# Performance work log

Measured on AMD Instinct MI355X. Metric: run time of the kernel, lower is better.

Reference implementation:

```python
import jax, jax.numpy as jnp
import numpy as np

HIDDEN = 2048
NUM_HEADS = 16
HEAD_DIM = 128
BLOCK_SIZE = 64
NUM_ACTIVE_BLOCKS = 4  # diagonal pattern -> bandwidth = 2 blocks each side
NEG_INF = -1e30  # stand-in for -inf that is safe under softmax in fp32


def _block_diagonal_additive_mask(seq_len: int) -> jnp.ndarray:
    """Token-level additive mask [S, S]; 0 where block |bi-bj|<=bandwidth, -inf else."""
    bandwidth = NUM_ACTIVE_BLOCKS // 2
    bid = jnp.arange(seq_len) // BLOCK_SIZE  # [S]
    active = jnp.abs(bid[:, None] - bid[None, :]) <= bandwidth  # [S, S] bool
    return jnp.where(active, 0.0, NEG_INF).astype(jnp.float32)


def setup_inputs() -> dict:
    key = jax.random.key(0)
    k0, k1, k2, k3, k4 = jax.random.split(key, 5)
    B, S = 2, 2048
    scale = 1.0 / np.sqrt(HIDDEN)
    return {
        "hidden_states": jax.random.normal(k0, (B, S, HIDDEN), dtype=jnp.float32),
        "Wq": jax.random.normal(k1, (HIDDEN, NUM_HEADS * HEAD_DIM), dtype=jnp.float32) * scale,
        "Wk": jax.random.normal(k2, (HIDDEN, NUM_HEADS * HEAD_DIM), dtype=jnp.float32) * scale,
        "Wv": jax.random.normal(k3, (HIDDEN, NUM_HEADS * HEAD_DIM), dtype=jnp.float32) * scale,
        "Wo": jax.random.normal(k4, (NUM_HEADS * HEAD_DIM, HIDDEN), dtype=jnp.float32) * scale,
    }


def reference(hidden_states, Wq, Wk, Wv, Wo):
    B, S, _ = hidden_states.shape
    scaling = HEAD_DIM ** -0.5

    # projections -> [B, H, S, D]
    def split_heads(x):
        return x.reshape(B, S, NUM_HEADS, HEAD_DIM).transpose(0, 2, 1, 3)

    q = split_heads(hidden_states @ Wq)
    k = split_heads(hidden_states @ Wk)
    v = split_heads(hidden_states @ Wv)

    mask = _block_diagonal_additive_mask(S)  # [S, S]

    # scores [B, H, S, S]
    scores = jnp.einsum("bhsd,bhtd->bhst", q, k) * scaling + mask[None, None]
    attn = jax.nn.softmax(scores.astype(jnp.float32), axis=-1).astype(q.dtype)

    out = jnp.einsum("bhst,bhtd->bhsd", attn, v)  # [B, H, S, D]
    out = out.transpose(0, 2, 1, 3).reshape(B, S, NUM_HEADS * HEAD_DIM)
    return out @ Wo
```

## Files before the change

kernel.cpp:

```cpp
#include <hip/hip_runtime.h>

typedef __attribute__((ext_vector_type(4))) float f32x4;
typedef __attribute__((ext_vector_type(16))) float f32x16;
typedef __attribute__((ext_vector_type(8))) _Float16 f16x8;
typedef __attribute__((ext_vector_type(4))) _Float16 f16x4;

__device__ __forceinline__ void gload_lds16(const void* g, void* l) {
  __builtin_amdgcn_global_load_lds((__attribute__((address_space(1))) void*)(g),
                                   (__attribute__((address_space(3))) void*)(l), 16, 0, 0);
}

#define BAR() asm volatile("s_barrier" ::: "memory")
#define WAITV8() asm volatile("s_waitcnt vmcnt(8)" ::: "memory")
#define WAITV6() asm volatile("s_waitcnt vmcnt(6)" ::: "memory")
#define WAITV4() asm volatile("s_waitcnt vmcnt(4)" ::: "memory")
#define WAITV0() asm volatile("s_waitcnt vmcnt(0)" ::: "memory")

__global__ __launch_bounds__(256) void prep(const float* __restrict__ Hs,
                                            const float* __restrict__ W0, const float* __restrict__ W1,
                                            const float* __restrict__ W2, const float* __restrict__ W3,
                                            _Float16* __restrict__ Hb, _Float16* __restrict__ Wt) {
  __shared__ _Float16 tile[64][65];
  const int bid = blockIdx.x, tid = threadIdx.x;
  if (bid < 8192) {
    int i = (bid * 256 + tid) * 4;
    float4 v = *(const float4*)(Hs + i);
    f16x4 o = { (_Float16)v.x, (_Float16)v.y, (_Float16)v.z, (_Float16)v.w };
    *(f16x4*)(Hb + i) = o;
    return;
  }
  const int t = bid - 8192;
  const int z = t >> 10, k0 = ((t >> 5) & 31) * 64, n0 = (t & 31) * 64;
  const float* W = z == 0 ? W0 : z == 1 ? W1 : z == 2 ? W2 : W3;
  _Float16* Wo_ = Wt + (size_t)z * (2048u * 2048u);
  #pragma unroll
  for (int p = 0; p < 4; ++p) {
    int o = p * 256 + tid, r = o >> 4, c = o & 15;
    float4 v = *(const float4*)(W + (size_t)(k0 + r) * 2048 + n0 + c * 4);
    tile[r][c * 4 + 0] = (_Float16)v.x;
    tile[r][c * 4 + 1] = (_Float16)v.y;
    tile[r][c * 4 + 2] = (_Float16)v.z;
    tile[r][c * 4 + 3] = (_Float16)v.w;
  }
  __syncthreads();
  #pragma unroll
  for (int p = 0; p < 2; ++p) {
    int o = p * 256 + tid, nl = o >> 3, c = o & 7;
    f16x8 u;
    #pragma unroll
    for (int i = 0; i < 8; ++i) u[i] = tile[c * 8 + i][nl];
    *(f16x8*)(Wo_ + (size_t)(n0 + nl) * 2048 + k0 + c * 8) = u;
  }
}

__device__ __forceinline__ void gemm256(const _Float16* __restrict__ A,
                                        const _Float16* __restrict__ Bt,
                                        _Float16* __restrict__ C, int ldc,
                                        int m0, int n0, _Float16* S) {
  _Float16* const As0 = S;
  _Float16* const As1 = S + 16384;
  _Float16* const Bs0 = S + 32768;
  _Float16* const Bs1 = S + 49152;
  const int tid = (int)threadIdx.x;
  const int lane = tid & 63, w = tid >> 6, l32 = lane & 31, half = lane >> 5;
  const int wm = (w & 1) * 128, wn = (w >> 1) * 64;

  f32x16 acc[4][2];
  #pragma unroll
  for (int s = 0; s < 4; ++s)
    #pragma unroll
    for (int t = 0; t < 2; ++t) acc[s][t] = 0;

  f16x8 af[2][4];
  f16x8 bf[2][4];

  auto stageA = [&](_Float16* dst, int ar, int kt) {
    const int r = tid >> 3, c = tid & 7;
    gload_lds16(A + (size_t)(m0 + ar + r) * 2048 + kt * 64 + ((c ^ (r & 7)) << 3),
                (char*)dst + ar * 128 + tid * 16);
  };
  auto stageB = [&](_Float16* dst, int br, int kt) {
    const int r = tid >> 3, c = tid & 7;
    gload_lds16(Bt + (size_t)(n0 + br + r) * 2048 + kt * 64 + ((c ^ (r & 7)) << 3),
                (char*)dst + br * 128 + tid * 16);
  };
  auto ldA = [&](const _Float16* as, int p) {
    #pragma unroll
    for (int s2 = 0; s2 < 2; ++s2)
      #pragma unroll
      for (int kk = 0; kk < 4; ++kk)
        af[s2][kk] = *(const f16x8*)(as + (wm + p * 64 + s2 * 32 + l32) * 64 +
                                     (((2 * kk + half) ^ (l32 & 7)) << 3));
  };
  auto ldB = [&](const _Float16* bs, int q) {
    #pragma unroll
    for (int kk = 0; kk < 4; ++kk)
      bf[q][kk] = *(const f16x8*)(bs + (wn + q * 32 + l32) * 64 +
                                  (((2 * kk + half) ^ (l32 & 7)) << 3));
  };
  auto mm8 = [&](int sp, int q) {
    __builtin_amdgcn_s_setprio(1);
    #pragma unroll
    for (int kk = 0; kk < 4; ++kk)
      #pragma unroll
      for (int s2 = 0; s2 < 2; ++s2)
        acc[sp * 2 + s2][q] = __builtin_amdgcn_mfma_f32_32x32x16_f16(
            bf[q][kk], af[s2][kk], acc[sp * 2 + s2][q], 0, 0, 0);
    __builtin_amdgcn_s_setprio(0);
  };

  stageA(As0, 0, 0); stageA(As0, 64, 0); stageA(As0, 128, 0); stageA(As0, 192, 0);
  stageB(Bs0, 0, 0); stageB(Bs0, 64, 0); stageB(Bs0, 128, 0); stageB(Bs0, 192, 0);
  stageA(As1, 0, 1); stageA(As1, 64, 1); stageA(As1, 128, 1); stageA(As1, 192, 1);
  stageB(Bs1, 0, 1); stageB(Bs1, 64, 1); stageB(Bs1, 128, 1); stageB(Bs1, 192, 1);
  WAITV8();
  BAR();

  auto tile = [&](int kt, _Float16* Ac, _Float16* Bc) {
    const bool g2 = (kt + 2) < 32;
    ldA(Ac, 0);
    ldB(Bc, 0); ldB(Bc, 1);
    mm8(0, 0);
    mm8(0, 1);
    ldA(Ac, 1);
    mm8(1, 1);
    mm8(1, 0);
    BAR();
    if (g2) {
      stageA(Ac, 0, kt + 2); stageA(Ac, 64, kt + 2);
      stageA(Ac, 128, kt + 2); stageA(Ac, 192, kt + 2);
      stageB(Bc, 0, kt + 2); stageB(Bc, 64, kt + 2);
      stageB(Bc, 128, kt + 2); stageB(Bc, 192, kt + 2);
      WAITV8();
    } else {
      WAITV0();
    }
    BAR();
  };

  #pragma unroll 1
  for (int kt = 0; kt < 32; kt += 2) {
    tile(kt, As0, Bs0);
    tile(kt + 1, As1, Bs1);
  }

  #pragma unroll
  for (int s = 0; s < 4; ++s) {
    const size_t row = (size_t)(wm + s * 32 + l32);
    #pragma unroll
    for (int t = 0; t < 2; ++t)
      #pragma unroll
      for (int g = 0; g < 4; ++g) {
        const int col = wn + t * 32 + g * 8 + 4 * half;
        f16x4 o = { (_Float16)acc[s][t][4 * g + 0], (_Float16)acc[s][t][4 * g + 1],
                    (_Float16)acc[s][t][4 * g + 2], (_Float16)acc[s][t][4 * g + 3] };
        *(f16x4*)(C + row * ldc + col) = o;
      }
  }
}

__device__ __forceinline__ void gemm128h(const _Float16* __restrict__ A,
                                         const _Float16* __restrict__ Bt,
                                         _Float16* __restrict__ C, int ldc,
                                         int m0, int n0, _Float16* S) {
  _Float16* const As0 = S;
  _Float16* const As1 = S + 8192;
  _Float16* const Bs0 = S + 16384;
  _Float16* const Bs1 = S + 32768;
  const int tid = (int)threadIdx.x;
  const int lane = tid & 63, w = tid >> 6, l32 = lane & 31, half = lane >> 5;
  const int wm = (w & 1) * 64, wn = (w >> 1) * 64;

  f32x16 acc[2][2];
  #pragma unroll
  for (int s = 0; s < 2; ++s)
    #pragma unroll
    for (int t = 0; t < 2; ++t) acc[s][t] = 0;

  f16x8 af[2][4], bf[2][4];

  auto stA = [&](_Float16* dst, int ar, int kt) {
    const int r = tid >> 3, c = tid & 7;
    gload_lds16(A + (size_t)(m0 + ar + r) * 2048 + kt * 64 + ((c ^ (r & 7)) << 3),
                (char*)dst + ar * 128 + tid * 16);
  };
  auto stB = [&](_Float16* dst, int br, int kt) {
    const int r = tid >> 3, c = tid & 7;
    gload_lds16(Bt + (size_t)(n0 + br + r) * 2048 + kt * 64 + ((c ^ (r & 7)) << 3),
                (char*)dst + br * 128 + tid * 16);
  };
  auto ldAq = [&](const _Float16* as) {
    #pragma unroll
    for (int s2 = 0; s2 < 2; ++s2)
      #pragma unroll
      for (int kk = 0; kk < 4; ++kk)
        af[s2][kk] = *(const f16x8*)(as + (wm + s2 * 32 + l32) * 64 +
                                     (((2 * kk + half) ^ (l32 & 7)) << 3));
  };
  auto ldBq = [&](const _Float16* bs, int q) {
    #pragma unroll
    for (int kk = 0; kk < 4; ++kk)
      bf[q][kk] = *(const f16x8*)(bs + (wn + q * 32 + l32) * 64 +
                                  (((2 * kk + half) ^ (l32 & 7)) << 3));
  };
  auto mmq = [&](int q) {
    __builtin_amdgcn_s_setprio(1);
    #pragma unroll
    for (int kk = 0; kk < 4; ++kk)
      #pragma unroll
      for (int s2 = 0; s2 < 2; ++s2)
        acc[s2][q] = __builtin_amdgcn_mfma_f32_32x32x16_f16(
            bf[q][kk], af[s2][kk], acc[s2][q], 0, 0, 0);
    __builtin_amdgcn_s_setprio(0);
  };

  stA(As0, 0, 0); stA(As0, 64, 0);
  stB(Bs0, 0, 0); stB(Bs0, 64, 0); stB(Bs0, 128, 0); stB(Bs0, 192, 0);
  stA(As1, 0, 1); stA(As1, 64, 1);
  stB(Bs1, 0, 1); stB(Bs1, 64, 1); stB(Bs1, 128, 1); stB(Bs1, 192, 1);
  WAITV6();
  BAR();

  auto tile = [&](int kt, _Float16* Ac, _Float16* Bc) {
    const bool g2 = (kt + 2) < 32;
    ldAq(Ac); ldBq(Bc, 0); ldBq(Bc, 1);
    mmq(0);
    mmq(1);
    BAR();
    if (g2) {
      stA(Ac, 0, kt + 2); stA(Ac, 64, kt + 2);
      stB(Bc, 0, kt + 2); stB(Bc, 64, kt + 2); stB(Bc, 128, kt + 2); stB(Bc, 192, kt + 2);
      WAITV6();
    } else {
      WAITV0();
    }
    BAR();
  };

  #pragma unroll 1
  for (int kt = 0; kt < 32; kt += 2) {
    tile(kt, As0, Bs0);
    tile(kt + 1, As1, Bs1);
  }

  #pragma unroll
  for (int s = 0; s < 2; ++s) {
    const size_t row = (size_t)(wm + s * 32 + l32);
    #pragma unroll
    for (int t = 0; t < 2; ++t)
      #pragma unroll
      for (int g = 0; g < 4; ++g) {
        const int col = wn + t * 32 + g * 8 + 4 * half;
        f16x4 o = { (_Float16)acc[s][t][4 * g + 0], (_Float16)acc[s][t][4 * g + 1],
                    (_Float16)acc[s][t][4 * g + 2], (_Float16)acc[s][t][4 * g + 3] };
        *(f16x4*)(C + row * ldc + col) = o;
      }
  }
}

__device__ __forceinline__ void gemm128f(const _Float16* __restrict__ A,
                                         const _Float16* __restrict__ Bt,
                                         float* __restrict__ C, int ldc,
                                         int m0, int n0, _Float16* S) {
  _Float16* const As0 = S;
  _Float16* const As1 = S + 8192;
  _Float16* const Bs0 = S + 16384;
  _Float16* const Bs1 = S + 32768;
  const int tid = (int)threadIdx.x;
  const int lane = tid & 63, w = tid >> 6, l32 = lane & 31, half = lane >> 5;
  const int wm = (w & 1) * 64, wn = (w >> 1) * 64;

  f32x16 acc[2][2];
  #pragma unroll
  for (int s = 0; s < 2; ++s)
    #pragma unroll
    for (int t = 0; t < 2; ++t) acc[s][t] = 0;

  f16x8 af[2][4], bf[2][4];

  auto stA = [&](_Float16* dst, int ar, int kt) {
    const int r = tid >> 3, c = tid & 7;
    gload_lds16(A + (size_t)(m0 + ar + r) * 2048 + kt * 64 + ((c ^ (r & 7)) << 3),
                (char*)dst + ar * 128 + tid * 16);
  };
  auto stB = [&](_Float16* dst, int br, int kt) {
    const int r = tid >> 3, c = tid & 7;
    gload_lds16(Bt + (size_t)(n0 + br + r) * 2048 + kt * 64 + ((c ^ (r & 7)) << 3),
                (char*)dst + br * 128 + tid * 16);
  };
  auto ldAq = [&](const _Float16* as) {
    #pragma unroll
    for (int s2 = 0; s2 < 2; ++s2)
      #pragma unroll
      for (int kk = 0; kk < 4; ++kk)
        af[s2][kk] = *(const f16x8*)(as + (wm + s2 * 32 + l32) * 64 +
                                     (((2 * kk + half) ^ (l32 & 7)) << 3));
  };
  auto ldBq = [&](const _Float16* bs, int q) {
    #pragma unroll
    for (int kk = 0; kk < 4; ++kk)
      bf[q][kk] = *(const f16x8*)(bs + (wn + q * 32 + l32) * 64 +
                                  (((2 * kk + half) ^ (l32 & 7)) << 3));
  };
  auto mmq = [&](int q) {
    __builtin_amdgcn_s_setprio(1);
    #pragma unroll
    for (int kk = 0; kk < 4; ++kk)
      #pragma unroll
      for (int s2 = 0; s2 < 2; ++s2)
        acc[s2][q] = __builtin_amdgcn_mfma_f32_32x32x16_f16(
            bf[q][kk], af[s2][kk], acc[s2][q], 0, 0, 0);
    __builtin_amdgcn_s_setprio(0);
  };

  stA(As0, 0, 0); stA(As0, 64, 0);
  stB(Bs0, 0, 0); stB(Bs0, 64, 0); stB(Bs0, 128, 0); stB(Bs0, 192, 0);
  stA(As1, 0, 1); stA(As1, 64, 1);
  stB(Bs1, 0, 1); stB(Bs1, 64, 1); stB(Bs1, 128, 1); stB(Bs1, 192, 1);
  WAITV6();
  BAR();

  auto tile = [&](int kt, _Float16* Ac, _Float16* Bc) {
    const bool g2 = (kt + 2) < 32;
    ldAq(Ac); ldBq(Bc, 0); ldBq(Bc, 1);
    mmq(0);
    mmq(1);
    BAR();
    if (g2) {
      stA(Ac, 0, kt + 2); stA(Ac, 64, kt + 2);
      stB(Bc, 0, kt + 2); stB(Bc, 64, kt + 2); stB(Bc, 128, kt + 2); stB(Bc, 192, kt + 2);
      WAITV6();
    } else {
      WAITV0();
    }
    BAR();
  };

  #pragma unroll 1
  for (int kt = 0; kt < 32; kt += 2) {
    tile(kt, As0, Bs0);
    tile(kt + 1, As1, Bs1);
  }

  #pragma unroll
  for (int s = 0; s < 2; ++s) {
    const size_t row = (size_t)(wm + s * 32 + l32);
    #pragma unroll
    for (int t = 0; t < 2; ++t)
      #pragma unroll
      for (int g = 0; g < 4; ++g) {
        const int col = wn + t * 32 + g * 8 + 4 * half;
        f32x4 o = { acc[s][t][4 * g + 0], acc[s][t][4 * g + 1],
                    acc[s][t][4 * g + 2], acc[s][t][4 * g + 3] };
        *(f32x4*)(C + row * ldc + col) = o;
      }
  }
}

__global__ __launch_bounds__(512, 2) void qkvv3(const _Float16* __restrict__ Hb,
                                                const _Float16* __restrict__ Wt,
                                                _Float16* __restrict__ Qb,
                                                _Float16* __restrict__ Kb,
                                                _Float16* __restrict__ Vtb) {
  __shared__ _Float16 S[65536];
  const int id = blockIdx.x;
  {
    const int m0 = (id >> 4) * 256, n0 = (id & 15) * 256;
    _Float16* Cq = (n0 < 2048 ? Qb + n0 : Kb + (n0 - 2048)) + (size_t)m0 * 2048;
    gemm256(Hb, Wt, Cq, 2048, m0, n0, S);
  }
  WAITV0();
  BAR();
  {
    const int m0 = (id >> 4) * 128, n0 = (id & 15) * 256;
    gemm128h(Wt + (size_t)2 * 4194304, Hb, Vtb + (size_t)m0 * 4096 + n0,
             4096, m0, n0, S);
  }
}

__global__ __launch_bounds__(512, 2) void gemm_wo(const _Float16* __restrict__ A,
                                                  const _Float16* __restrict__ Bt,
                                                  float* __restrict__ C) {
  __shared__ _Float16 S[49152];
  const int t = blockIdx.x;
  const int m0 = (t >> 3) * 128, n0 = (t & 7) * 256;
  gemm128f(A, Bt, C + (size_t)m0 * 2048 + n0, 2048, m0, n0, S);
}

__global__ __launch_bounds__(256) void attn(const _Float16* __restrict__ Qg,
                                            const _Float16* __restrict__ Kg,
                                            const _Float16* __restrict__ Vtg,
                                            _Float16* __restrict__ Og) {
  const int t = blockIdx.x, h = blockIdx.y, b = blockIdx.z;
  __shared__ _Float16 Qs[128 * 128];
  __shared__ _Float16 Ks[64 * 128];
  __shared__ _Float16 Vs[128 * 64];
  const int tid = threadIdx.x;
  const int lane = tid & 63, w = tid >> 6, l16 = lane & 15, quad = lane >> 4;
  const int qbw = 2 * t + (w >> 1);
  const char* QsB = (const char*)Qs;
  const char* KsB = (const char*)Ks;
  const char* VsB = (const char*)Vs;

  #pragma unroll
  for (int p = 0; p < 8; ++p) {
    int o = p * 256 + tid, r = o >> 4, c = o & 15;
    gload_lds16(Qg + (size_t)(b * 2048 + t * 128 + r) * 2048 + h * 128 + ((c ^ (r & 15)) * 8),
                (char*)Qs + o * 16);
  }
  __builtin_amdgcn_s_waitcnt(0);
  __syncthreads();
  f16x8 qf[2][4];
  #pragma unroll
  for (int qc = 0; qc < 2; ++qc)
    #pragma unroll
    for (int ks = 0; ks < 4; ++ks)
      qf[qc][ks] = *(const f16x8*)(QsB + (w * 32 + qc * 16 + l16) * 256 +
                                   (((ks * 4 + quad) ^ l16) * 16));

  const float scale = 0.08838834764831845f;
  float m_[2] = {-1e30f, -1e30f}, l_[2] = {0.f, 0.f};
  f32x4 oacc[8][2];
  #pragma unroll
  for (int dt = 0; dt < 8; ++dt)
    #pragma unroll
    for (int qc = 0; qc < 2; ++qc) oacc[dt][qc] = (f32x4){0.f, 0.f, 0.f, 0.f};

  for (int jj = 0; jj < 6; ++jj) {
    const int j = 2 * t - 2 + jj;
    const int jc = j < 0 ? 0 : (j > 31 ? 31 : j);
    __syncthreads();
    #pragma unroll
    for (int p = 0; p < 4; ++p) {
      int o = p * 256 + tid, r = o >> 4, c = o & 15;
      gload_lds16(Kg + (size_t)(b * 2048 + jc * 64 + r) * 2048 + h * 128 + ((c ^ (r & 15)) * 8),
                  (char*)Ks + o * 16);
    }
    #pragma unroll
    for (int p = 0; p < 4; ++p) {
      int o = p * 256 + tid, d = o >> 3, c = o & 7;
      gload_lds16(Vtg + (size_t)(h * 128 + d) * 4096 + b * 2048 + jc * 64 + ((c ^ (d & 7)) * 8),
                  (char*)Vs + o * 16);
    }
    WAITV4();
    BAR();

    const bool valid = (j >= 0) && (j <= 31) && (j >= qbw - 2) && (j <= qbw + 2);
    f32x4 sc[4][2];
    f16x4 pb[4][2];
    if (valid) {
      #pragma unroll
      for (int kt = 0; kt < 4; ++kt)
        #pragma unroll
        for (int qc = 0; qc < 2; ++qc) sc[kt][qc] = (f32x4){0.f, 0.f, 0.f, 0.f};
      #pragma unroll
      for (int kt = 0; kt < 4; ++kt)
        #pragma unroll
        for (int ks = 0; ks < 4; ++ks) {
          f16x8 kf = *(const f16x8*)(KsB + (kt * 16 + l16) * 256 + (((ks * 4 + quad) ^ l16) * 16));
          #pragma unroll
          for (int qc = 0; qc < 2; ++qc)
            sc[kt][qc] = __builtin_amdgcn_mfma_f32_16x16x32_f16(kf, qf[qc][ks], sc[kt][qc], 0, 0, 0);
        }
      #pragma unroll
      for (int qc = 0; qc < 2; ++qc) {
        float mj = -1e30f;
        #pragma unroll
        for (int kt = 0; kt < 4; ++kt)
          #pragma unroll
          for (int r = 0; r < 4; ++r) {
            float v = sc[kt][qc][r] * scale;
            sc[kt][qc][r] = v;
            mj = fmaxf(mj, v);
          }
        mj = fmaxf(mj, __shfl_xor(mj, 16));
        mj = fmaxf(mj, __shfl_xor(mj, 32));
        const float mn = fmaxf(m_[qc], mj);
        const float alpha = __expf(m_[qc] - mn);
        float s_ = 0.f;
        #pragma unroll
        for (int kt = 0; kt < 4; ++kt)
          #pragma unroll
          for (int r = 0; r < 4; ++r) {
            float p = __expf(sc[kt][qc][r] - mn);
            sc[kt][qc][r] = p;
            s_ += p;
          }
        s_ += __shfl_xor(s_, 16);
        s_ += __shfl_xor(s_, 32);
        l_[qc] = l_[qc] * alpha + s_;
        m_[qc] = mn;
        #pragma unroll
        for (int dt = 0; dt < 8; ++dt) oacc[dt][qc] *= alpha;
      }
      #pragma unroll
      for (int kt = 0; kt < 4; ++kt)
        #pragma unroll
        for (int qc = 0; qc < 2; ++qc)
          pb[kt][qc] = (f16x4){ (_Float16)sc[kt][qc][0], (_Float16)sc[kt][qc][1],
                                (_Float16)sc[kt][qc][2], (_Float16)sc[kt][qc][3] };
    }
    WAITV0();
    BAR();
    if (valid) {
      #pragma unroll
      for (int kt = 0; kt < 4; ++kt) {
        #pragma unroll
        for (int dt = 0; dt < 8; ++dt) {
          f16x4 vv = *(const f16x4*)(VsB + (dt * 16 + l16) * 128 +
                                     (((2 * kt + (quad >> 1)) ^ (l16 & 7)) * 16) + (quad & 1) * 8);
          #pragma unroll
          for (int qc = 0; qc < 2; ++qc)
            oacc[dt][qc] = __builtin_amdgcn_mfma_f32_16x16x16f16(vv, pb[kt][qc], oacc[dt][qc], 0, 0, 0);
        }
      }
    }
  }

  #pragma unroll
  for (int qc = 0; qc < 2; ++qc) {
    const float pinv = 1.0f / l_[qc];
    const size_t orow = (size_t)(b * 2048 + t * 128 + w * 32 + qc * 16 + l16);
    #pragma unroll
    for (int dt = 0; dt < 8; ++dt) {
      f16x4 ov = { (_Float16)(oacc[dt][qc][0] * pinv), (_Float16)(oacc[dt][qc][1] * pinv),
                   (_Float16)(oacc[dt][qc][2] * pinv), (_Float16)(oacc[dt][qc][3] * pinv) };
      *(f16x4*)(Og + orow * 2048 + h * 128 + dt * 16 + quad * 4) = ov;
    }
  }
}

extern "C" void kernel_launch(void* const* d_in, const int* in_sizes, int n_in,
                              void* d_out, int out_size, void* d_ws, size_t ws_size,
                              hipStream_t stream) {
  const float* Hs = (const float*)d_in[0];
  const float* Wq = (const float*)d_in[1];
  const float* Wk = (const float*)d_in[2];
  const float* Wv = (const float*)d_in[3];
  const float* Wo = (const float*)d_in[4];
  _Float16* Hb  = (_Float16*)d_ws;
  _Float16* Wt  = Hb  + 8388608;
  _Float16* Qb  = Wt  + 16777216;
  _Float16* Kb  = Qb  + 8388608;
  _Float16* Vtb = Kb  + 8388608;
  _Float16* Ob  = Vtb + 8388608;
  float* out = (float*)d_out;

  prep<<<12288, 256, 0, stream>>>(Hs, Wq, Wk, Wv, Wo, Hb, Wt);
  qkvv3<<<256, 512, 0, stream>>>(Hb, Wt, Qb, Kb, Vtb);
  attn<<<dim3(16, 16, 2), 256, 0, stream>>>(Qb, Kb, Vtb, Ob);
  gemm_wo<<<256, 512, 0, stream>>>(Ob, Wt + (size_t)3 * 4194304, out);
}
```

Before: 343.8 us.

## Split QKV kernel and rewrite QK GEMM with 16x16 MFMA finer-grained pipeline

Replaces the fused QKV kernel with two launches: a new Q/K GEMM kernel and a separate V-transpose GEMM kernel. The Q/K GEMM switches from 32x32x16 to 16x16x32 MFMA fragments and restructures the main loop into eight interleaved phases, each staging a slice of the next tile's global-to-LDS loads before its quarter of the MFMAs, with barriers and lgkmcnt waits around each phase. The aim is to spread the global loads across the compute and hide their latency better. The cost is many more barriers per k-step, and splitting the kernel adds a launch and removes the intra-kernel reuse of the workgroup.

Result: faster. 334.7 us (-2.7%).

```diff
diff --git a/kernel.cpp b/kernel.cpp
--- a/kernel.cpp
+++ b/kernel.cpp
@@ -11,7 +11,7 @@
 }
 
 #define BAR() asm volatile("s_barrier" ::: "memory")
-#define WAITV8() asm volatile("s_waitcnt vmcnt(8)" ::: "memory")
+#define LGKM0() asm volatile("s_waitcnt lgkmcnt(0)" ::: "memory")
 #define WAITV6() asm volatile("s_waitcnt vmcnt(6)" ::: "memory")
 #define WAITV4() asm volatile("s_waitcnt vmcnt(4)" ::: "memory")
 #define WAITV0() asm volatile("s_waitcnt vmcnt(0)" ::: "memory")
@@ -53,109 +53,134 @@
   }
 }
 
-__device__ __forceinline__ void gemm256(const _Float16* __restrict__ A,
-                                        const _Float16* __restrict__ Bt,
-                                        _Float16* __restrict__ C, int ldc,
-                                        int m0, int n0, _Float16* S) {
+__global__ __launch_bounds__(512, 2) void qk8(const _Float16* __restrict__ A,
+                                              const _Float16* __restrict__ Bt,
+                                              _Float16* __restrict__ Qb,
+                                              _Float16* __restrict__ Kb) {
+  __shared__ _Float16 S[65536];
   _Float16* const As0 = S;
   _Float16* const As1 = S + 16384;
   _Float16* const Bs0 = S + 32768;
   _Float16* const Bs1 = S + 49152;
+
+  const int id = blockIdx.x;
+  const int m0 = (id >> 4) * 256, n0 = (id & 15) * 256;
+  _Float16* const C = (n0 < 2048 ? Qb + n0 : Kb + (n0 - 2048)) + (size_t)m0 * 2048;
+  const int ldc = 2048;
+
   const int tid = (int)threadIdx.x;
-  const int lane = tid & 63, w = tid >> 6, l32 = lane & 31, half = lane >> 5;
+  const int lane = tid & 63, w = tid >> 6, l16 = lane & 15, quad = lane >> 4;
   const int wm = (w & 1) * 128, wn = (w >> 1) * 64;
 
-  f32x16 acc[4][2];
-  #pragma unroll
-  for (int s = 0; s < 4; ++s)
-    #pragma unroll
-    for (int t = 0; t < 2; ++t) acc[s][t] = 0;
-
-  f16x8 af[2][4];
-  f16x8 bf[2][4];
-
-  auto stageA = [&](_Float16* dst, int ar, int kt) {
+  f32x4 acc[8][4];
+  #pragma unroll
+  for (int fm = 0; fm < 8; ++fm)
+    #pragma unroll
+    for (int fn = 0; fn < 4; ++fn) acc[fm][fn] = (f32x4){0.f, 0.f, 0.f, 0.f};
+
+  f16x8 af[4][2];
+  f16x8 bf[2][2][2];
+
+  auto stA = [&](_Float16* dst, int ar, int kt) {
     const int r = tid >> 3, c = tid & 7;
     gload_lds16(A + (size_t)(m0 + ar + r) * 2048 + kt * 64 + ((c ^ (r & 7)) << 3),
                 (char*)dst + ar * 128 + tid * 16);
   };
-  auto stageB = [&](_Float16* dst, int br, int kt) {
+  auto stB = [&](_Float16* dst, int br, int kt) {
     const int r = tid >> 3, c = tid & 7;
     gload_lds16(Bt + (size_t)(n0 + br + r) * 2048 + kt * 64 + ((c ^ (r & 7)) << 3),
                 (char*)dst + br * 128 + tid * 16);
   };
-  auto ldA = [&](const _Float16* as, int p) {
-    #pragma unroll
-    for (int s2 = 0; s2 < 2; ++s2)
-      #pragma unroll
-      for (int kk = 0; kk < 4; ++kk)
-        af[s2][kk] = *(const f16x8*)(as + (wm + p * 64 + s2 * 32 + l32) * 64 +
-                                     (((2 * kk + half) ^ (l32 & 7)) << 3));
-  };
-  auto ldB = [&](const _Float16* bs, int q) {
-    #pragma unroll
-    for (int kk = 0; kk < 4; ++kk)
-      bf[q][kk] = *(const f16x8*)(bs + (wn + q * 32 + l32) * 64 +
-                                  (((2 * kk + half) ^ (l32 & 7)) << 3));
-  };
-  auto mm8 = [&](int sp, int q) {
+  auto ldA = [&](const _Float16* as, int qm) {
+    #pragma unroll
+    for (int fm = 0; fm < 4; ++fm)
+      #pragma unroll
+      for (int ks = 0; ks < 2; ++ks)
+        af[fm][ks] = *(const f16x8*)(as + (wm + qm * 64 + fm * 16 + l16) * 64 +
+                                     (((ks * 4 + quad) ^ (l16 & 7)) << 3));
+  };
+  auto ldB = [&](const _Float16* bs, int qn) {
+    #pragma unroll
+    for (int fn = 0; fn < 2; ++fn)
+      #pragma unroll
+      for (int ks = 0; ks < 2; ++ks)
+        bf[qn][fn][ks] = *(const f16x8*)(bs + (wn + qn * 32 + fn * 16 + l16) * 64 +
+                                         (((ks * 4 + quad) ^ (l16 & 7)) << 3));
+  };
+  auto mm16 = [&](int qm, int qn) {
     __builtin_amdgcn_s_setprio(1);
     #pragma unroll
-    for (int kk = 0; kk < 4; ++kk)
-      #pragma unroll
-      for (int s2 = 0; s2 < 2; ++s2)
-        acc[sp * 2 + s2][q] = __builtin_amdgcn_mfma_f32_32x32x16_f16(
-            bf[q][kk], af[s2][kk], acc[sp * 2 + s2][q], 0, 0, 0);
+    for (int ks = 0; ks < 2; ++ks)
+      #pragma unroll
+      for (int fm = 0; fm < 4; ++fm)
+        #pragma unroll
+        for (int fn = 0; fn < 2; ++fn)
+          acc[qm * 4 + fm][qn * 2 + fn] = __builtin_amdgcn_mfma_f32_16x16x32_f16(
+              bf[qn][fn][ks], af[fm][ks], acc[qm * 4 + fm][qn * 2 + fn], 0, 0, 0);
     __builtin_amdgcn_s_setprio(0);
   };
 
-  stageA(As0, 0, 0); stageA(As0, 64, 0); stageA(As0, 128, 0); stageA(As0, 192, 0);
-  stageB(Bs0, 0, 0); stageB(Bs0, 64, 0); stageB(Bs0, 128, 0); stageB(Bs0, 192, 0);
-  stageA(As1, 0, 1); stageA(As1, 64, 1); stageA(As1, 128, 1); stageA(As1, 192, 1);
-  stageB(Bs1, 0, 1); stageB(Bs1, 64, 1); stageB(Bs1, 128, 1); stageB(Bs1, 192, 1);
-  WAITV8();
+  stA(As0, 0, 0); stA(As0, 64, 0); stA(As0, 128, 0); stA(As0, 192, 0);
+  stB(Bs0, 0, 0); stB(Bs0, 64, 0); stB(Bs0, 128, 0); stB(Bs0, 192, 0);
+  stA(As1, 0, 1); stA(As1, 128, 1);
+  stB(Bs1, 0, 1); stB(Bs1, 64, 1); stB(Bs1, 128, 1); stB(Bs1, 192, 1);
+  WAITV6();
   BAR();
 
-  auto tile = [&](int kt, _Float16* Ac, _Float16* Bc) {
-    const bool g2 = (kt + 2) < 32;
-    ldA(Ac, 0);
-    ldB(Bc, 0); ldB(Bc, 1);
-    mm8(0, 0);
-    mm8(0, 1);
-    ldA(Ac, 1);
-    mm8(1, 1);
-    mm8(1, 0);
-    BAR();
-    if (g2) {
-      stageA(Ac, 0, kt + 2); stageA(Ac, 64, kt + 2);
-      stageA(Ac, 128, kt + 2); stageA(Ac, 192, kt + 2);
-      stageB(Bc, 0, kt + 2); stageB(Bc, 64, kt + 2);
-      stageB(Bc, 128, kt + 2); stageB(Bc, 192, kt + 2);
-      WAITV8();
-    } else {
-      WAITV0();
-    }
-    BAR();
-  };
-
   #pragma unroll 1
-  for (int kt = 0; kt < 32; kt += 2) {
-    tile(kt, As0, Bs0);
-    tile(kt + 1, As1, Bs1);
-  }
-
-  #pragma unroll
-  for (int s = 0; s < 4; ++s) {
-    const size_t row = (size_t)(wm + s * 32 + l32);
-    #pragma unroll
-    for (int t = 0; t < 2; ++t)
-      #pragma unroll
-      for (int g = 0; g < 4; ++g) {
-        const int col = wn + t * 32 + g * 8 + 4 * half;
-        f16x4 o = { (_Float16)acc[s][t][4 * g + 0], (_Float16)acc[s][t][4 * g + 1],
-                    (_Float16)acc[s][t][4 * g + 2], (_Float16)acc[s][t][4 * g + 3] };
-        *(f16x4*)(C + row * ldc + col) = o;
-      }
+  for (int I = 0; I < 16; ++I) {
+    const int t1 = 2 * I + 1, t2 = 2 * I + 2, t3 = 2 * I + 3;
+    const bool g2 = t2 < 32, g3 = t3 < 32;
+    ldA(As0, 0); ldB(Bs0, 0);
+    stA(As1, 64, t1); stA(As1, 192, t1);
+    BAR(); LGKM0();
+    mm16(0, 0);
+    BAR();
+    ldB(Bs0, 1);
+    if (g2) { stA(As0, 0, t2); stA(As0, 128, t2); }
+    BAR(); LGKM0();
+    mm16(0, 1);
+    BAR();
+    ldA(As0, 1);
+    if (g2) { stB(Bs0, 0, t2); stB(Bs0, 64, t2); }
+    BAR(); LGKM0();
+    mm16(1, 1);
+    BAR();
+    if (g2) { stB(Bs0, 128, t2); stB(Bs0, 192, t2); WAITV6(); } else { WAITV0(); }
+    BAR(); LGKM0();
+    mm16(1, 0);
+    BAR();
+    ldA(As1, 0); ldB(Bs1, 0);
+    if (g2) { stA(As0, 64, t2); stA(As0, 192, t2); }
+    BAR(); LGKM0();
+    mm16(0, 0);
+    BAR();
+    ldB(Bs1, 1);
+    if (g3) { stA(As1, 0, t3); stA(As1, 128, t3); }
+    BAR(); LGKM0();
+    mm16(0, 1);
+    BAR();
+    ldA(As1, 1);
+    if (g3) { stB(Bs1, 0, t3); stB(Bs1, 64, t3); }
+    BAR(); LGKM0();
+    mm16(1, 1);
+    BAR();
+    if (g3) { stB(Bs1, 128, t3); stB(Bs1, 192, t3); WAITV6(); } else { WAITV0(); }
+    BAR(); LGKM0();
+    mm16(1, 0);
+    BAR();
+  }
+
+  #pragma unroll
+  for (int fm = 0; fm < 8; ++fm) {
+    const size_t row = (size_t)(wm + fm * 16 + l16);
+    #pragma unroll
+    for (int fn = 0; fn < 4; ++fn) {
+      const int col = wn + fn * 16 + quad * 4;
+      f16x4 o = { (_Float16)acc[fm][fn][0], (_Float16)acc[fm][fn][1],
+                  (_Float16)acc[fm][fn][2], (_Float16)acc[fm][fn][3] };
+      *(f16x4*)(C + row * ldc + col) = o;
+    }
   }
 }
 
@@ -357,25 +382,13 @@
   }
 }
 
-__global__ __launch_bounds__(512, 2) void qkvv3(const _Float16* __restrict__ Hb,
-                                                const _Float16* __restrict__ Wt,
-                                                _Float16* __restrict__ Qb,
-                                                _Float16* __restrict__ Kb,
-                                                _Float16* __restrict__ Vtb) {
-  __shared__ _Float16 S[65536];
+__global__ __launch_bounds__(512, 2) void vt(const _Float16* __restrict__ Hb,
+                                             const _Float16* __restrict__ WvT,
+                                             _Float16* __restrict__ Vtb) {
+  __shared__ _Float16 S[49152];
   const int id = blockIdx.x;
-  {
-    const int m0 = (id >> 4) * 256, n0 = (id & 15) * 256;
-    _Float16* Cq = (n0 < 2048 ? Qb + n0 : Kb + (n0 - 2048)) + (size_t)m0 * 2048;
-    gemm256(Hb, Wt, Cq, 2048, m0, n0, S);
-  }
-  WAITV0();
-  BAR();
-  {
-    const int m0 = (id >> 4) * 128, n0 = (id & 15) * 256;
-    gemm128h(Wt + (size_t)2 * 4194304, Hb, Vtb + (size_t)m0 * 4096 + n0,
-             4096, m0, n0, S);
-  }
+  const int m0 = (id >> 4) * 128, n0 = (id & 15) * 256;
+  gemm128h(WvT, Hb, Vtb + (size_t)m0 * 4096 + n0, 4096, m0, n0, S);
 }
 
 __global__ __launch_bounds__(512, 2) void gemm_wo(const _Float16* __restrict__ A,
@@ -547,7 +560,8 @@
   float* out = (float*)d_out;
 
   prep<<<12288, 256, 0, stream>>>(Hs, Wq, Wk, Wv, Wo, Hb, Wt);
-  qkvv3<<<256, 512, 0, stream>>>(Hb, Wt, Qb, Kb, Vtb);
+  qk8<<<256, 512, 0, stream>>>(Hb, Wt, Qb, Kb);
+  vt<<<256, 512, 0, stream>>>(Hb, Wt + (size_t)2 * 4194304, Vtb);
   attn<<<dim3(16, 16, 2), 256, 0, stream>>>(Qb, Kb, Vtb, Ob);
   gemm_wo<<<256, 512, 0, stream>>>(Ob, Wt + (size_t)3 * 4194304, out);
 }
```
